# Performance work log

Measured on AMD Instinct MI355X. Metric: run time of the kernel, lower is better.

Reference implementation:

```python
import jax, jax.numpy as jnp
import numpy as np

BN_EPS = 1e-5

def _conv3x3(x, w):
    # x: [N,C,H,W], w: [O,I,3,3], stride 1, padding 1, no bias
    return jax.lax.conv_general_dilated(
        x, w, window_strides=(1, 1), padding=((1, 1), (1, 1)),
        dimension_numbers=("NCHW", "OIHW", "NCHW"))

def _batchnorm(x, gamma, beta):
    # training-mode BN: batch statistics over (N,H,W)
    mean = jnp.mean(x, axis=(0, 2, 3), keepdims=True)
    var = jnp.mean(jnp.square(x - mean), axis=(0, 2, 3), keepdims=True)
    inv = jax.lax.rsqrt(var + BN_EPS)
    g = gamma.reshape(1, -1, 1, 1)
    b = beta.reshape(1, -1, 1, 1)
    return (x - mean) * inv * g + b

def setup_inputs() -> dict:
    key = jax.random.key(0)
    ks = jax.random.split(key, 3)
    x = jax.random.normal(ks[0], (32, 64, 128, 128), dtype=jnp.float32)
    # He-style scaled 3x3 conv kernels
    w1 = jax.random.normal(ks[1], (64, 64, 3, 3), dtype=jnp.float32) * (2.0 / (64 * 9)) ** 0.5
    w2 = jax.random.normal(ks[2], (64, 64, 3, 3), dtype=jnp.float32) * (2.0 / (64 * 9)) ** 0.5
    return {
        "x": x, "w1": w1, "w2": w2,
        "bn1_gamma": jnp.ones((64,), jnp.float32),
        "bn1_beta": jnp.zeros((64,), jnp.float32),
        "bn2_gamma": jnp.ones((64,), jnp.float32),
        "bn2_beta": jnp.zeros((64,), jnp.float32),
    }

def reference(x, w1, w2, bn1_gamma, bn1_beta, bn2_gamma, bn2_beta):
    out = _batchnorm(_conv3x3(x, w1), bn1_gamma, bn1_beta)
    out = _conv3x3(out, w2)
    out = out + x  # option 'A', stride=1, planes[2]==planes[0] -> identity shortcut
    return _batchnorm(out, bn2_gamma, bn2_beta)
```

## Files before the change

### kernel.cpp

```cpp
#include <hip/hip_runtime.h>
#include <hip/hip_bf16.h>

#define NB 32
#define CH 64
#define HH 128
#define WW 128
#define HW (HH*WW)
#define CHW (CH*HW)
#define NCHW (NB*CHW)
#define CNT_PER_CH ((float)(NB*HW))

typedef __attribute__((ext_vector_type(8)))  short short8;
typedef __attribute__((ext_vector_type(16))) float f32x16;

__device__ __forceinline__ unsigned short f2bf(float f) {
  unsigned u = __builtin_bit_cast(unsigned, f);
  u += 0x7fffu + ((u >> 16) & 1u);
  return (unsigned short)(u >> 16);
}

__device__ __forceinline__ void gld_lds16(const void* g, void* s) {
  __builtin_amdgcn_global_load_lds(
      (const __attribute__((address_space(1))) unsigned int*)g,
      (__attribute__((address_space(3))) unsigned int*)s, 16, 0, 0);
}

__global__ __launch_bounds__(256) void t1_pack(const float* __restrict__ x,
                                               unsigned short* __restrict__ xb) {
  __shared__ __align__(16) unsigned short tmp[CH * WW];
  const int bid = blockIdx.x;
  const int tid = threadIdx.x;
  const float* src = x + (size_t)(bid >> 7) * CHW + (size_t)(bid & 127) * WW;
  for (int i = tid; i < 2048; i += 256) {
    const int ci = i >> 5, wq = i & 31;
    const float4 v = *(const float4*)(src + (size_t)ci * HW + wq * 4);
    unsigned short* d = &tmp[ci * WW + wq * 4];
    d[0] = f2bf(v.x); d[1] = f2bf(v.y); d[2] = f2bf(v.z); d[3] = f2bf(v.w);
  }
  __syncthreads();
  unsigned short* dst = xb + (size_t)bid * 8192;
  for (int i = tid; i < 1024; i += 256) {
    const int cb = i >> 7, w = i & 127;
    const unsigned short* s = &tmp[cb * 8 * WW + w];
    uint4 o;
    o.x = (unsigned)s[0]      | ((unsigned)s[WW]     << 16);
    o.y = (unsigned)s[2*WW]   | ((unsigned)s[3*WW]   << 16);
    o.z = (unsigned)s[4*WW]   | ((unsigned)s[5*WW]   << 16);
    o.w = (unsigned)s[6*WW]   | ((unsigned)s[7*WW]   << 16);
    *(uint4*)(dst + ((size_t)cb * WW + w) * 8) = o;
  }
}

__global__ __launch_bounds__(256) void pack_w(const float* __restrict__ w,
                                              const float* __restrict__ s1,
                                              const float* __restrict__ b1,
                                              unsigned short* __restrict__ wpk,
                                              float* __restrict__ tabs) {
  const int tid = threadIdx.x;
  for (int idx = tid; idx < 36864; idx += 256) {
    const int f = idx >> 9, l = (idx >> 3) & 63, r = idx & 7;
    const int m = f & 1, kq = (f >> 1) & 3, t = f >> 3;
    const int co = (l & 31) + 32 * m;
    const int ci = kq * 16 + (l >> 5) * 8 + r;
    float v = w[co * 576 + ci * 9 + t];
    if (s1) v *= s1[ci];
    wpk[idx] = f2bf(v);
  }
  if (tabs != nullptr && tid < 64) {
    const int co = tid;
    float tb[9];
    for (int t = 0; t < 9; ++t) {
      float a = 0.f;
      for (int ci = 0; ci < 64; ++ci) a += w[co * 576 + ci * 9 + t] * b1[ci];
      tb[t] = a;
    }
    tabs[0*64+co] = tb[0]+tb[1]+tb[2]+tb[3]+tb[4]+tb[5]+tb[6]+tb[7]+tb[8];
    tabs[1*64+co] = tb[0]+tb[1]+tb[2];
    tabs[2*64+co] = tb[6]+tb[7]+tb[8];
    tabs[3*64+co] = tb[0]+tb[3]+tb[6];
    tabs[4*64+co] = tb[2]+tb[5]+tb[8];
    tabs[5*64+co] = tb[0]; tabs[6*64+co] = tb[2];
    tabs[7*64+co] = tb[6]; tabs[8*64+co] = tb[8];
  }
}

template <bool IS2>
__global__ __launch_bounds__(256)
void conv_mfma(const unsigned short* __restrict__ inb,
               const unsigned short* __restrict__ wpack,
               const float* __restrict__ tabs,
               const float* __restrict__ resid,
               unsigned short* __restrict__ outb,
               float* __restrict__ outf,
               float* __restrict__ psum, float* __restrict__ psq) {
  __shared__ __align__(16) unsigned short A[3 * 8 * 132 * 8];
  const int tid = threadIdx.x, bid = blockIdx.x;
  const int n = bid >> 7, h = bid & 127;
  const int wv = tid >> 6, lane = tid & 63;
  const int half = lane >> 5, lp = lane & 31;
  const int wb = wv * 32;

  if (tid < 48) {
    const int r = tid >> 4, cb = (tid & 15) >> 1, s = (tid & 1) ? 129 : 0;
    *(uint4*)&A[((r * 8 + cb) * 132 + s) * 8] = make_uint4(0, 0, 0, 0);
  }
  for (int q = wv; q < 48; q += 4) {
    const int r = q >> 4, cb = (q & 15) >> 1, hf = q & 1;
    const int hr = h - 1 + r;
    if ((unsigned)hr < 128u) {
      const unsigned short* g =
          inb + ((((size_t)n * 128 + hr) * 8 + cb) * 128 + hf * 64) * 8 + (size_t)lane * 8;
      gld_lds16(g, &A[((r * 8 + cb) * 132 + 1 + hf * 64) * 8]);
    }
  }
  __syncthreads();

  f32x16 acc0 = {}; f32x16 acc1 = {};
  const int kh0 = (h == 0) ? 1 : 0;
  const int kh1 = (h == 127) ? 1 : 2;
  for (int kh = kh0; kh <= kh1; ++kh) {
    for (int kw = 0; kw < 3; ++kw) {
#pragma unroll
      for (int kq = 0; kq < 4; ++kq) {
        const short8 bfrag =
            *(const short8*)&A[((kh * 8 + kq * 2 + half) * 132 + (wb + lp + kw)) * 8];
        const int f = ((kh * 3 + kw) * 4 + kq) * 2;
        const short8 w0 = *(const short8*)(wpack + (size_t)f * 512 + lane * 8);
        const short8 w1 = *(const short8*)(wpack + (size_t)(f + 1) * 512 + lane * 8);
        acc0 = __builtin_amdgcn_mfma_f32_32x32x16_bf16(w0, bfrag, acc0, 0, 0, 0);
        acc1 = __builtin_amdgcn_mfma_f32_32x32x16_bf16(w1, bfrag, acc1, 0, 0, 0);
      }
    }
  }

  if (!IS2) {
    unsigned short* dst = outb + (size_t)bid * 8192;
#pragma unroll
    for (int m = 0; m < 2; ++m) {
      const f32x16& a = m ? acc1 : acc0;
#pragma unroll
      for (int q = 0; q < 4; ++q) {
        uint2 pk;
        pk.x = (unsigned)f2bf(a[q*4+0]) | ((unsigned)f2bf(a[q*4+1]) << 16);
        pk.y = (unsigned)f2bf(a[q*4+2]) | ((unsigned)f2bf(a[q*4+3]) << 16);
        *(uint2*)(dst + ((size_t)(q + 4*m) * 128 + wb + lp) * 8 + half * 4) = pk;
      }
    }
  } else {
    const int w = wb + lp;
    const bool bh0 = (h == 0), bh1 = (h == 127);
    const bool bw0 = (w == 0), bw1 = (w == 127);
#pragma unroll
    for (int m = 0; m < 2; ++m) {
      f32x16& a = m ? acc1 : acc0;
#pragma unroll
      for (int q = 0; q < 4; ++q) {
#pragma unroll
        for (int j = 0; j < 4; ++j) {
          const int co = j + 8*q + 4*half + 32*m;
          float v = a[q*4+j];
          float tb = tabs[co];
          if (bh0) tb -= tabs[64 + co];
          if (bh1) tb -= tabs[128 + co];
          if (bw0) tb -= tabs[192 + co];
          if (bw1) tb -= tabs[256 + co];
          if (bh0 && bw0) tb += tabs[320 + co];
          if (bh0 && bw1) tb += tabs[384 + co];
          if (bh1 && bw0) tb += tabs[448 + co];
          if (bh1 && bw1) tb += tabs[512 + co];
          v += tb;
          const size_t oi = (((size_t)n * 64 + co) * HW) + (size_t)h * WW + w;
          v += resid[oi];
          outf[oi] = v;
          a[q*4+j] = v;
        }
      }
    }
  }

  __syncthreads();
  float* sf = (float*)A;
#pragma unroll
  for (int m = 0; m < 2; ++m) {
    const f32x16& a = m ? acc1 : acc0;
#pragma unroll
    for (int q = 0; q < 4; ++q)
#pragma unroll
      for (int j = 0; j < 4; ++j)
        sf[(j + 8*q + 4*half + 32*m) * 128 + wb + lp] = a[q*4+j];
  }
  __syncthreads();
  {
    const int co = tid >> 2, qt = tid & 3;
    const float* p = &sf[co * 128 + qt * 32];
    float s = 0.f, q2 = 0.f;
#pragma unroll
    for (int i = 0; i < 32; i += 4) {
      const float4 v = *(const float4*)&p[i];
      s  += v.x + v.y + v.z + v.w;
      q2 += v.x*v.x + v.y*v.y + v.z*v.z + v.w*v.w;
    }
    s  += __shfl_xor(s, 1);  s  += __shfl_xor(s, 2);
    q2 += __shfl_xor(q2, 1); q2 += __shfl_xor(q2, 2);
    if (qt == 0) {
      atomicAdd(&psum[(bid & 63) * 64 + co], s);
      atomicAdd(&psq [(bid & 63) * 64 + co], q2);
    }
  }
}

__global__ void finalize_bn(const float* __restrict__ psum, const float* __restrict__ psq,
                            const float* __restrict__ gamma, const float* __restrict__ beta,
                            float* __restrict__ scale, float* __restrict__ bias) {
  const int c = threadIdx.x;
  if (c < 64) {
    float s = 0.f, q = 0.f;
    for (int i = 0; i < 64; ++i) { s += psum[i * 64 + c]; q += psq[i * 64 + c]; }
    const float mean = s * (1.0f / CNT_PER_CH);
    const float var  = q * (1.0f / CNT_PER_CH) - mean * mean;
    const float inv  = rsqrtf(var + 1e-5f);
    const float sc   = inv * gamma[c];
    scale[c] = sc;
    bias[c]  = beta[c] - mean * sc;
  }
}

__global__ __launch_bounds__(256)
void apply_bn_k(float* __restrict__ out,
                const float* __restrict__ scale, const float* __restrict__ bias) {
  __shared__ float sc[CH], bs[CH];
  if (threadIdx.x < CH) { sc[threadIdx.x] = scale[threadIdx.x]; bs[threadIdx.x] = bias[threadIdx.x]; }
  __syncthreads();
  const size_t total4 = NCHW / 4;
  for (size_t i = (size_t)blockIdx.x * blockDim.x + threadIdx.x; i < total4;
       i += (size_t)gridDim.x * blockDim.x) {
    float4 v = reinterpret_cast<float4*>(out)[i];
    const int c = (int)(((i * 4) >> 14) & 63);
    const float s = sc[c], b = bs[c];
    v.x = fmaf(v.x, s, b);
    v.y = fmaf(v.y, s, b);
    v.z = fmaf(v.z, s, b);
    v.w = fmaf(v.w, s, b);
    reinterpret_cast<float4*>(out)[i] = v;
  }
}

extern "C" void kernel_launch(void* const* d_in, const int* in_sizes, int n_in,
                              void* d_out, int out_size, void* d_ws, size_t ws_size,
                              hipStream_t stream) {
  const float* x  = (const float*)d_in[0];
  const float* w1 = (const float*)d_in[1];
  const float* w2 = (const float*)d_in[2];
  const float* g1 = (const float*)d_in[3];
  const float* b1 = (const float*)d_in[4];
  const float* g2 = (const float*)d_in[5];
  const float* b2 = (const float*)d_in[6];
  float* out = (float*)d_out;
  char* ws = (char*)d_ws;

  unsigned short* XB  = (unsigned short*)ws;
  unsigned short* Y1B = (unsigned short*)(ws + 67108864);
  unsigned short* W2P = (unsigned short*)ws;
  float* TABS = (float*)(ws + 73728);
  float* SC1  = (float*)(ws + 76032);
  float* BS1  = (float*)(ws + 76288);
  float* SC2  = (float*)(ws + 76544);
  float* BS2  = (float*)(ws + 76800);
  float* P2S  = (float*)(ws + 77056);
  float* P2Q  = (float*)(ws + 93440);
  char* ob = (char*)d_out;
  unsigned short* W1P = (unsigned short*)ob;
  float* P1S = (float*)(ob + 73728);
  float* P1Q = (float*)(ob + 90112);

  hipMemsetAsync(ob + 73728, 0, 32768, stream);
  pack_w<<<1, 256, 0, stream>>>(w1, nullptr, nullptr, W1P, nullptr);
  t1_pack<<<4096, 256, 0, stream>>>(x, XB);
  conv_mfma<false><<<4096, 256, 0, stream>>>(XB, W1P, nullptr, nullptr,
                                             Y1B, nullptr, P1S, P1Q);
  finalize_bn<<<1, 64, 0, stream>>>(P1S, P1Q, g1, b1, SC1, BS1);
  hipMemsetAsync(ws + 77056, 0, 32768, stream);
  pack_w<<<1, 256, 0, stream>>>(w2, SC1, BS1, W2P, TABS);
  conv_mfma<true><<<4096, 256, 0, stream>>>(Y1B, W2P, TABS, x,
                                            nullptr, out, P2S, P2Q);
  finalize_bn<<<1, 64, 0, stream>>>(P2S, P2Q, g2, b2, SC2, BS2);
  apply_bn_k<<<2048, 256, 0, stream>>>(out, SC2, BS2);
}
```

Before: 538.2 us.

## Keep conv weights in registers and split waves over output-channel and pixel tiles

Each wave now owns one 32-channel half of the outputs and two 32-pixel tiles. Its 36 weight fragments are preloaded into registers instead of being re-read from global memory inside the MFMA loop. Out-of-range halo rows are zero-filled so the kh loop is fully unrolled. The BN statistics reduction moves from an LDS transpose plus barriers to in-register wave shuffles, and launch bounds request two blocks per CU. The trade-off is higher register pressure from holding weights, which may cause spills, and the extra atomics issued per wave.

```diff
diff --git a/kernel.cpp b/kernel.cpp
--- a/kernel.cpp
+++ b/kernel.cpp
@@ -85,7 +85,7 @@
 }
 
 template <bool IS2>
-__global__ __launch_bounds__(256)
+__global__ __launch_bounds__(256, 2)
 void conv_mfma(const unsigned short* __restrict__ inb,
                const unsigned short* __restrict__ wpack,
                const float* __restrict__ tabs,
@@ -93,118 +93,109 @@
                unsigned short* __restrict__ outb,
                float* __restrict__ outf,
                float* __restrict__ psum, float* __restrict__ psq) {
-  __shared__ __align__(16) unsigned short A[3 * 8 * 132 * 8];
+  __shared__ __align__(16) unsigned short A[3][8][130][8];
   const int tid = threadIdx.x, bid = blockIdx.x;
   const int n = bid >> 7, h = bid & 127;
   const int wv = tid >> 6, lane = tid & 63;
   const int half = lane >> 5, lp = lane & 31;
-  const int wb = wv * 32;
-
-  if (tid < 48) {
-    const int r = tid >> 4, cb = (tid & 15) >> 1, s = (tid & 1) ? 129 : 0;
-    *(uint4*)&A[((r * 8 + cb) * 132 + s) * 8] = make_uint4(0, 0, 0, 0);
-  }
+  const int m  = wv & 1;
+  const int nb = (wv >> 1) << 1;
+
   for (int q = wv; q < 48; q += 4) {
-    const int r = q >> 4, cb = (q & 15) >> 1, hf = q & 1;
-    const int hr = h - 1 + r;
+    const int rr = q >> 4, cb = (q >> 1) & 7, w0 = (q & 1) << 6;
+    const int hr = h - 1 + rr;
     if ((unsigned)hr < 128u) {
       const unsigned short* g =
-          inb + ((((size_t)n * 128 + hr) * 8 + cb) * 128 + hf * 64) * 8 + (size_t)lane * 8;
-      gld_lds16(g, &A[((r * 8 + cb) * 132 + 1 + hf * 64) * 8]);
-    }
+          inb + ((((size_t)n * 128 + hr) * 8 + cb) << 10) + (size_t)(w0 + lane) * 8;
+      gld_lds16(g, &A[rr][cb][1 + w0][0]);
+    } else {
+      *(uint4*)&A[rr][cb][1 + w0 + lane][0] = make_uint4(0, 0, 0, 0);
+    }
+  }
+  if (tid < 48) {
+    const int rr = tid >> 4, cb = (tid >> 1) & 7, s = (tid & 1) ? 129 : 0;
+    *(uint4*)&A[rr][cb][s][0] = make_uint4(0, 0, 0, 0);
+  }
+
+  short8 wr[36];
+#pragma unroll
+  for (int i = 0; i < 36; ++i) {
+    const int f = ((i >> 2) << 3) + ((i & 3) << 1) + m;
+    wr[i] = *(const short8*)(wpack + (size_t)f * 512 + (size_t)lane * 8);
   }
   __syncthreads();
 
   f32x16 acc0 = {}; f32x16 acc1 = {};
-  const int kh0 = (h == 0) ? 1 : 0;
-  const int kh1 = (h == 127) ? 1 : 2;
-  for (int kh = kh0; kh <= kh1; ++kh) {
+#pragma unroll
+  for (int kh = 0; kh < 3; ++kh) {
+#pragma unroll
     for (int kw = 0; kw < 3; ++kw) {
 #pragma unroll
       for (int kq = 0; kq < 4; ++kq) {
-        const short8 bfrag =
-            *(const short8*)&A[((kh * 8 + kq * 2 + half) * 132 + (wb + lp + kw)) * 8];
-        const int f = ((kh * 3 + kw) * 4 + kq) * 2;
-        const short8 w0 = *(const short8*)(wpack + (size_t)f * 512 + lane * 8);
-        const short8 w1 = *(const short8*)(wpack + (size_t)(f + 1) * 512 + lane * 8);
-        acc0 = __builtin_amdgcn_mfma_f32_32x32x16_bf16(w0, bfrag, acc0, 0, 0, 0);
-        acc1 = __builtin_amdgcn_mfma_f32_32x32x16_bf16(w1, bfrag, acc1, 0, 0, 0);
+        const short8 wf = wr[(kh * 3 + kw) * 4 + kq];
+        const int cb = kq * 2 + half;
+        const short8 b0 = *(const short8*)&A[kh][cb][nb * 32 + lp + kw][0];
+        const short8 b1 = *(const short8*)&A[kh][cb][(nb + 1) * 32 + lp + kw][0];
+        acc0 = __builtin_amdgcn_mfma_f32_32x32x16_bf16(wf, b0, acc0, 0, 0, 0);
+        acc1 = __builtin_amdgcn_mfma_f32_32x32x16_bf16(wf, b1, acc1, 0, 0, 0);
       }
     }
   }
 
   if (!IS2) {
-    unsigned short* dst = outb + (size_t)bid * 8192;
-#pragma unroll
-    for (int m = 0; m < 2; ++m) {
-      const f32x16& a = m ? acc1 : acc0;
-#pragma unroll
-      for (int q = 0; q < 4; ++q) {
+    unsigned short* dst = outb + ((size_t)bid << 13);
+#pragma unroll
+    for (int nt = 0; nt < 2; ++nt) {
+      const f32x16& a = nt ? acc1 : acc0;
+      const int px = (nb + nt) * 32 + lp;
+#pragma unroll
+      for (int rq = 0; rq < 4; ++rq) {
         uint2 pk;
-        pk.x = (unsigned)f2bf(a[q*4+0]) | ((unsigned)f2bf(a[q*4+1]) << 16);
-        pk.y = (unsigned)f2bf(a[q*4+2]) | ((unsigned)f2bf(a[q*4+3]) << 16);
-        *(uint2*)(dst + ((size_t)(q + 4*m) * 128 + wb + lp) * 8 + half * 4) = pk;
+        pk.x = (unsigned)f2bf(a[rq*4+0]) | ((unsigned)f2bf(a[rq*4+1]) << 16);
+        pk.y = (unsigned)f2bf(a[rq*4+2]) | ((unsigned)f2bf(a[rq*4+3]) << 16);
+        *(uint2*)(dst + (((size_t)(rq + 4*m)) << 10) + (size_t)px * 8 + half * 4) = pk;
       }
     }
   } else {
-    const int w = wb + lp;
     const bool bh0 = (h == 0), bh1 = (h == 127);
-    const bool bw0 = (w == 0), bw1 = (w == 127);
-#pragma unroll
-    for (int m = 0; m < 2; ++m) {
-      f32x16& a = m ? acc1 : acc0;
-#pragma unroll
-      for (int q = 0; q < 4; ++q) {
-#pragma unroll
-        for (int j = 0; j < 4; ++j) {
-          const int co = j + 8*q + 4*half + 32*m;
-          float v = a[q*4+j];
-          float tb = tabs[co];
-          if (bh0) tb -= tabs[64 + co];
-          if (bh1) tb -= tabs[128 + co];
-          if (bw0) tb -= tabs[192 + co];
-          if (bw1) tb -= tabs[256 + co];
-          if (bh0 && bw0) tb += tabs[320 + co];
-          if (bh0 && bw1) tb += tabs[384 + co];
-          if (bh1 && bw0) tb += tabs[448 + co];
-          if (bh1 && bw1) tb += tabs[512 + co];
-          v += tb;
-          const size_t oi = (((size_t)n * 64 + co) * HW) + (size_t)h * WW + w;
-          v += resid[oi];
-          outf[oi] = v;
-          a[q*4+j] = v;
-        }
+#pragma unroll
+    for (int nt = 0; nt < 2; ++nt) {
+      f32x16& a = nt ? acc1 : acc0;
+      const int px = (nb + nt) * 32 + lp;
+      const bool bw0 = (px == 0), bw1 = (px == 127);
+#pragma unroll
+      for (int r = 0; r < 16; ++r) {
+        const int co = (r & 3) + ((r >> 2) << 3) + 4 * half + 32 * m;
+        float tb = tabs[co];
+        if (bh0) tb -= tabs[64 + co];
+        if (bh1) tb -= tabs[128 + co];
+        if (bw0) tb -= tabs[192 + co];
+        if (bw1) tb -= tabs[256 + co];
+        if (bh0 && bw0) tb += tabs[320 + co];
+        if (bh0 && bw1) tb += tabs[384 + co];
+        if (bh1 && bw0) tb += tabs[448 + co];
+        if (bh1 && bw1) tb += tabs[512 + co];
+        const size_t oi = (((size_t)n * 64 + co) * 128 + h) * 128 + px;
+        const float v = a[r] + tb + resid[oi];
+        outf[oi] = v;
+        a[r] = v;
       }
     }
   }
 
-  __syncthreads();
-  float* sf = (float*)A;
-#pragma unroll
-  for (int m = 0; m < 2; ++m) {
-    const f32x16& a = m ? acc1 : acc0;
-#pragma unroll
-    for (int q = 0; q < 4; ++q)
-#pragma unroll
-      for (int j = 0; j < 4; ++j)
-        sf[(j + 8*q + 4*half + 32*m) * 128 + wb + lp] = a[q*4+j];
-  }
-  __syncthreads();
-  {
-    const int co = tid >> 2, qt = tid & 3;
-    const float* p = &sf[co * 128 + qt * 32];
-    float s = 0.f, q2 = 0.f;
-#pragma unroll
-    for (int i = 0; i < 32; i += 4) {
-      const float4 v = *(const float4*)&p[i];
-      s  += v.x + v.y + v.z + v.w;
-      q2 += v.x*v.x + v.y*v.y + v.z*v.z + v.w*v.w;
-    }
-    s  += __shfl_xor(s, 1);  s  += __shfl_xor(s, 2);
-    q2 += __shfl_xor(q2, 1); q2 += __shfl_xor(q2, 2);
-    if (qt == 0) {
+#pragma unroll
+  for (int r = 0; r < 16; ++r) {
+    float s = acc0[r] + acc1[r];
+    float q = acc0[r] * acc0[r] + acc1[r] * acc1[r];
+    s += __shfl_xor(s, 1);  q += __shfl_xor(q, 1);
+    s += __shfl_xor(s, 2);  q += __shfl_xor(q, 2);
+    s += __shfl_xor(s, 4);  q += __shfl_xor(q, 4);
+    s += __shfl_xor(s, 8);  q += __shfl_xor(q, 8);
+    s += __shfl_xor(s, 16); q += __shfl_xor(q, 16);
+    if (lp == 0) {
+      const int co = (r & 3) + ((r >> 2) << 3) + 4 * half + 32 * m;
       atomicAdd(&psum[(bid & 63) * 64 + co], s);
-      atomicAdd(&psq [(bid & 63) * 64 + co], q2);
+      atomicAdd(&psq [(bid & 63) * 64 + co], q);
     }
   }
 }
```

Result: slower. 575.0 us (+6.8%).
